# Kernel tuning notes

Hardware: AMD Instinct MI355X
Metric: run time of the kernel (lower is better)

The kernel has to match this reference:

```python
import jax, jax.numpy as jnp
import numpy as np

B, L, C, EW, H = 4, 512, 512, 64, 8
D = C // H          # dot_dim = 64
NI = 1024           # node ffn inner = round(512*2.0)
EI = 64             # edge ffn inner = round(64*1.0)
CLIP_LO, CLIP_HI = -5.0, 5.0


def _ln(x, g, b):
    m = jnp.mean(x, -1, keepdims=True)
    v = jnp.var(x, -1, keepdims=True)
    return (x - m) * jax.lax.rsqrt(v + 1e-5) * g + b


def setup_inputs() -> dict:
    key = jax.random.key(0)
    ks = iter(jax.random.split(key, 16))
    nrm = lambda shp: (0.02 * jax.random.normal(next(ks), shp)).astype(jnp.float32)
    z = lambda n: jnp.zeros((n,), jnp.float32)
    o = lambda n: jnp.ones((n,), jnp.float32)
    return {
        'h': jax.random.normal(next(ks), (B, L, C), jnp.float32),
        'e': jax.random.normal(next(ks), (B, L, L, EW), jnp.float32),
        'ln_h_g': o(C), 'ln_h_b': z(C),
        'ln_e_g': o(EW), 'ln_e_b': z(EW),
        'W_QKV': nrm((C, 3 * C)), 'b_QKV': z(3 * C),
        'W_E': nrm((EW, H)), 'b_E': z(H),
        'W_G': nrm((EW, H)), 'b_G': z(H),
        'W_Oh': nrm((C, C)), 'b_Oh': z(C),
        'ffn_ln_h_g': o(C), 'ffn_ln_h_b': z(C),
        'W_h1': nrm((C, NI)), 'b_h1': z(NI),
        'W_h2': nrm((NI, C)), 'b_h2': z(C),
        'W_Oe': nrm((H, EW)), 'b_Oe': z(EW),
        'ffn_ln_e_g': o(EW), 'ffn_ln_e_b': z(EW),
        'W_e1': nrm((EW, EI)), 'b_e1': z(EI),
        'W_e2': nrm((EI, EW)), 'b_e2': z(EW),
    }


def reference(h, e, ln_h_g, ln_h_b, ln_e_g, ln_e_b, W_QKV, b_QKV, W_E, b_E,
              W_G, b_G, W_Oh, b_Oh, ffn_ln_h_g, ffn_ln_h_b, W_h1, b_h1,
              W_h2, b_h2, W_Oe, b_Oe, ffn_ln_e_g, ffn_ln_e_b, W_e1, b_e1,
              W_e2, b_e2):
    h_ln = _ln(h, ln_h_g, ln_h_b)
    e_ln = _ln(e, ln_e_g, ln_e_b)
    QKV = h_ln @ W_QKV + b_QKV                    # [B,L,3C]
    E = e_ln @ W_E + b_E                          # [B,L,L,H]
    G = e_ln @ W_G + b_G                          # [B,L,L,H]
    qkv = QKV.reshape(B, L, 3 * D, H)             # torch view(B,L,-1,H)
    Q, K, V = qkv[:, :, :D], qkv[:, :, D:2 * D], qkv[:, :, 2 * D:]
    A_hat = jnp.einsum('bldh,bmdh->blmh', Q, K) * (D ** -0.5)
    H_hat = jnp.clip(A_hat, CLIP_LO, CLIP_HI) + E  # [B,L,L,H]
    gates = jax.nn.sigmoid(G)
    A_tild = jax.nn.softmax(H_hat, axis=2) * gates
    V_att = jnp.einsum('blmh,bmkh->blkh', A_tild, V)  # [B,L,D,H]
    deg = jnp.log1p(jnp.sum(gates, axis=2, keepdims=True))  # [B,L,1,H]
    V_att = (V_att * deg).reshape(B, L, C)
    # node MHA residual + FFN
    h1 = V_att @ W_Oh + b_Oh + h
    h_f = _ln(h1, ffn_ln_h_g, ffn_ln_h_b)
    h_out = h1 + (jax.nn.elu(h_f @ W_h1 + b_h1) @ W_h2 + b_h2)
    # edge MHA residual + FFN
    e1 = H_hat @ W_Oe + b_Oe + e
    e_f = _ln(e1, ffn_ln_e_g, ffn_ln_e_b)
    e_out = e1 + (jax.nn.elu(e_f @ W_e1 + b_e1) @ W_e2 + b_e2)
    return (h_out, e_out)
```

## Files before the change

### kernel.cpp

```cpp
#include <hip/hip_runtime.h>
#include <math.h>

typedef unsigned short u16t;
typedef unsigned int   u32t;
typedef __bf16 bf16x8 __attribute__((ext_vector_type(8)));
typedef float  f32x4  __attribute__((ext_vector_type(4)));

#define DEV static __device__ __forceinline__

DEV u16t bfc(float x){ u32t b=__float_as_uint(x); b += 0x7FFFu + ((b>>16)&1u); return (u16t)(b>>16); }
DEV float flc(u16t u){ return __uint_as_float(((u32t)u)<<16); }
DEV u32t pk2(u16t a, u16t b){ return (u32t)a | ((u32t)b<<16); }
DEV f32x4 fz4(){ f32x4 z = {0.f,0.f,0.f,0.f}; return z; }
DEV bf16x8 bz8(){ uint4 z = make_uint4(0u,0u,0u,0u); return __builtin_bit_cast(bf16x8, z); }
DEV f32x4 MFMA(bf16x8 a, bf16x8 b, f32x4 c){ return __builtin_amdgcn_mfma_f32_16x16x32_bf16(a,b,c,0,0,0); }

__global__ void kwTall(const float* __restrict__ A, u16t* __restrict__ oA,
                       const float* __restrict__ B, u16t* __restrict__ oB,
                       const float* __restrict__ C, u16t* __restrict__ oC,
                       const float* __restrict__ D, u16t* __restrict__ oD){
  int id = blockIdx.x*256 + threadIdx.x;
  if (id < 786432){ int n=id>>9, k=id&511; oA[id]=bfc(A[(size_t)k*1536+n]); return; }
  id -= 786432;
  if (id < 262144){ int n=id>>9, k=id&511; int ks=(k&63)*8+(k>>6); oB[id]=bfc(B[(size_t)ks*512+n]); return; }
  id -= 262144;
  if (id < 524288){ int n=id>>9, k=id&511; oC[id]=bfc(C[(size_t)k*1024+n]); return; }
  id -= 524288;
  { int n=id>>10, k=id&1023; oD[id]=bfc(D[(size_t)k*512+n]); }
}

__global__ __launch_bounds__(256) void kln(const float* __restrict__ in, const float* __restrict__ g,
                                           const float* __restrict__ b, u16t* __restrict__ out){
  int wv = threadIdx.x >> 6, lane = threadIdx.x & 63;
  int row = blockIdx.x*4 + wv;
  const float4* rp = reinterpret_cast<const float4*>(in + (size_t)row*512);
  float4 v0 = rp[lane], v1 = rp[lane+64];
  float s = v0.x+v0.y+v0.z+v0.w + v1.x+v1.y+v1.z+v1.w;
  float q = v0.x*v0.x+v0.y*v0.y+v0.z*v0.z+v0.w*v0.w + v1.x*v1.x+v1.y*v1.y+v1.z*v1.z+v1.w*v1.w;
  #pragma unroll
  for (int m=1;m<64;m<<=1){ s += __shfl_xor(s,m); q += __shfl_xor(q,m); }
  float mean = s*(1.f/512.f), var = q*(1.f/512.f)-mean*mean, rs = rsqrtf(var+1e-5f);
  const float4* gp = reinterpret_cast<const float4*>(g);
  const float4* bp = reinterpret_cast<const float4*>(b);
  float4 g0=gp[lane], g1=gp[lane+64], b0=bp[lane], b1=bp[lane+64];
  u16t* op = out + (size_t)row*512;
  ushort4 o0 = make_ushort4(bfc((v0.x-mean)*rs*g0.x+b0.x), bfc((v0.y-mean)*rs*g0.y+b0.y),
                            bfc((v0.z-mean)*rs*g0.z+b0.z), bfc((v0.w-mean)*rs*g0.w+b0.w));
  ushort4 o1 = make_ushort4(bfc((v1.x-mean)*rs*g1.x+b1.x), bfc((v1.y-mean)*rs*g1.y+b1.y),
                            bfc((v1.z-mean)*rs*g1.z+b1.z), bfc((v1.w-mean)*rs*g1.w+b1.w));
  reinterpret_cast<ushort4*>(op)[lane]    = o0;
  reinterpret_cast<ushort4*>(op)[lane+64] = o1;
}

__global__ __launch_bounds__(256) void kqkv(const u16t* __restrict__ hln, const u16t* __restrict__ Wt,
    const float* __restrict__ bias, u16t* __restrict__ Qb, u16t* __restrict__ Kb, u16t* __restrict__ Vt)
{
  __shared__ __align__(16) u16t As[16][520];
  __shared__ __align__(16) u16t Cs[16][1024];
  const int r0 = blockIdx.x*16, t = threadIdx.x;
  const int b8 = (r0 >> 9) * 8, pos0 = r0 & 511;
  {
    int row = t>>4, seg = t&15;
    const uint4* src = reinterpret_cast<const uint4*>(hln + (size_t)(r0+row)*512 + seg*32);
    uint4* dst = reinterpret_cast<uint4*>(&As[row][seg*32]);
    dst[0]=src[0]; dst[1]=src[1]; dst[2]=src[2]; dst[3]=src[3];
  }
  __syncthreads();
  const int wv = t>>6, lane = t&63;
  const int frow = lane&15, kgrp = (lane>>4)*8, rbase = (lane>>4)*4;
  for (int nt=0; nt<24; nt++){
    int n0 = (wv*24+nt)*16;
    f32x4 acc = fz4();
    for (int k0=0;k0<512;k0+=32){
      bf16x8 af = *reinterpret_cast<const bf16x8*>(&As[frow][k0+kgrp]);
      bf16x8 bf_ = *reinterpret_cast<const bf16x8*>(Wt + (size_t)(n0+frow)*512 + k0+kgrp);
      acc = MFMA(af,bf_,acc);
    }
    int col = n0 + frow;
    float bs = bias[col];
    if (n0 < 1024){
      #pragma unroll
      for (int r=0;r<4;r++) Cs[rbase+r][col] = bfc(acc[r]+bs);
    } else {
      int cc = col - 1024, dv = cc>>3, hq = cc&7;
      ushort4 u4 = make_ushort4(bfc(acc[0]+bs), bfc(acc[1]+bs), bfc(acc[2]+bs), bfc(acc[3]+bs));
      *reinterpret_cast<ushort4*>(Vt + ((size_t)(b8+hq)*64 + dv)*512 + pos0 + rbase) = u4;
    }
  }
  __syncthreads();
  {
    int pair = t>>1, halfq = t&1;
    int hq = pair>>4, lq = pair&15, d0 = halfq*32;
    int pos = pos0 + lq;
    u16t* qdst = Qb + ((size_t)(b8+hq)*512 + pos)*64 + d0;
    u16t* kdst = Kb + ((size_t)(b8+hq)*512 + pos)*64 + d0;
    #pragma unroll
    for (int v2=0; v2<4; v2++){
      uint4 u, uk;
      u.x  = pk2(Cs[lq][(d0+v2*8+0)*8+hq], Cs[lq][(d0+v2*8+1)*8+hq]);
      u.y  = pk2(Cs[lq][(d0+v2*8+2)*8+hq], Cs[lq][(d0+v2*8+3)*8+hq]);
      u.z  = pk2(Cs[lq][(d0+v2*8+4)*8+hq], Cs[lq][(d0+v2*8+5)*8+hq]);
      u.w  = pk2(Cs[lq][(d0+v2*8+6)*8+hq], Cs[lq][(d0+v2*8+7)*8+hq]);
      uk.x = pk2(Cs[lq][512+(d0+v2*8+0)*8+hq], Cs[lq][512+(d0+v2*8+1)*8+hq]);
      uk.y = pk2(Cs[lq][512+(d0+v2*8+2)*8+hq], Cs[lq][512+(d0+v2*8+3)*8+hq]);
      uk.z = pk2(Cs[lq][512+(d0+v2*8+4)*8+hq], Cs[lq][512+(d0+v2*8+5)*8+hq]);
      uk.w = pk2(Cs[lq][512+(d0+v2*8+6)*8+hq], Cs[lq][512+(d0+v2*8+7)*8+hq]);
      reinterpret_cast<uint4*>(qdst)[v2] = u;
      reinterpret_cast<uint4*>(kdst)[v2] = uk;
    }
  }
}

__global__ __launch_bounds__(512,4) void kattnF(
    const float* __restrict__ e, const float* __restrict__ lng, const float* __restrict__ lnb,
    const float* __restrict__ WE, const float* __restrict__ bE,
    const float* __restrict__ WG, const float* __restrict__ bG,
    const u16t* __restrict__ Qb, const u16t* __restrict__ Kb,
    const float* __restrict__ WOe, const float* __restrict__ bOe,
    const float* __restrict__ flg, const float* __restrict__ flb,
    const float* __restrict__ We1, const float* __restrict__ be1,
    const float* __restrict__ We2, const float* __restrict__ be2,
    u16t* __restrict__ Pg, float* __restrict__ Sp, float* __restrict__ Dp,
    float* __restrict__ eout)
{
  __shared__ __align__(16) u16t Eln[256][72];
  __shared__ u16t EGb[256][18];
  __shared__ __align__(16) u16t Hl[256][8];
  __shared__ __align__(16) u16t Pgs[16][8][16];
  __shared__ __align__(16) u16t WEGt[16][72];
  __shared__ __align__(16) u16t We1t[64][72];
  __shared__ __align__(16) u16t We2t[64][72];
  __shared__ __align__(16) u16t WOeT[64][8];
  __shared__ float lgs[64], lbs[64], flgs[64], flbs[64], bOes[64], be1s[64], be2s[64];
  __shared__ float bEs[8], bGs[8];

  const int t = threadIdx.x;
  const int b = blockIdx.z, lblk = blockIdx.x, chunk = blockIdx.y;
  const int l0 = lblk*16, m0g = chunk*128, b8 = b*8;

  if (t < 64){
    lgs[t]=lng[t]; lbs[t]=lnb[t]; flgs[t]=flg[t]; flbs[t]=flb[t];
    bOes[t]=bOe[t]; be1s[t]=be1[t]; be2s[t]=be2[t];
  }
  if (t < 8){ bEs[t]=bE[t]; bGs[t]=bG[t]; }
  for (int i=t; i<16*64; i+=512){
    int n = i>>6, k = i&63;
    WEGt[n][k] = bfc(n<8 ? WE[k*8+n] : WG[k*8+(n-8)]);
  }
  for (int i=t; i<4096; i+=512){
    int n=i>>6, k=i&63;
    We1t[n][k] = bfc(We1[k*64+n]);
    We2t[n][k] = bfc(We2[k*64+n]);
  }
  for (int i=t; i<512; i+=512){
    int n=i>>3, hh=i&7;
    WOeT[n][hh] = bfc(WOe[hh*64+n]);
  }
  __syncthreads();

  const int wv = t>>6, lane = t&63;
  const int frow = lane&15, kgrp = (lane>>4)*8, rbase = (lane>>4)*4;

  bf16x8 qf[2];
  #pragma unroll
  for (int kk=0;kk<2;kk++)
    qf[kk] = *reinterpret_cast<const bf16x8*>(Qb + ((size_t)(b8+wv)*512 + l0+frow)*64 + kk*32 + kgrp);

  float Ssum[4] = {0.f,0.f,0.f,0.f}, Dsum[4] = {0.f,0.f,0.f,0.f};

  const float* ebs[2];
  #pragma unroll
  for (int ti=0; ti<2; ti++)
    ebs[ti] = e + ((size_t)((b*512 + l0 + 2*wv+ti)*512) + m0g + frow)*64 + rbase;

  float4 xr[2][4];
  #pragma unroll
  for (int ti=0; ti<2; ti++)
    #pragma unroll
    for (int nb=0; nb<4; nb++)
      xr[ti][nb] = *reinterpret_cast<const float4*>(ebs[ti] + nb*16);

  #pragma unroll 1
  for (int mt=0; mt<8; mt++){
    const int m0 = m0g + mt*16;
    #pragma unroll
    for (int ti=0; ti<2; ti++){
      const int T = 2*wv + ti;
      float s_=0.f, q_=0.f;
      #pragma unroll
      for (int nb=0; nb<4; nb++){
        float4 v = xr[ti][nb];
        s_ += v.x+v.y+v.z+v.w;
        q_ += v.x*v.x+v.y*v.y+v.z*v.z+v.w*v.w;
      }
      s_ += __shfl_xor(s_,16); q_ += __shfl_xor(q_,16);
      s_ += __shfl_xor(s_,32); q_ += __shfl_xor(q_,32);
      float mean = s_*(1.f/64.f), var = q_*(1.f/64.f)-mean*mean, rs = rsqrtf(var+1e-5f);
      #pragma unroll
      for (int nb=0; nb<4; nb++){
        int n = nb*16 + rbase;
        float4 v = xr[ti][nb];
        uint2 uv;
        uv.x = pk2(bfc((v.x-mean)*rs*lgs[n  ]+lbs[n  ]), bfc((v.y-mean)*rs*lgs[n+1]+lbs[n+1]));
        uv.y = pk2(bfc((v.z-mean)*rs*lgs[n+2]+lbs[n+2]), bfc((v.w-mean)*rs*lgs[n+3]+lbs[n+3]));
        *reinterpret_cast<uint2*>(&Eln[T*16+frow][n]) = uv;
      }
    }
    #pragma unroll
    for (int ti=0; ti<2; ti++){
      int T = wv*2+ti;
      bf16x8 a0 = *reinterpret_cast<const bf16x8*>(&Eln[T*16+frow][kgrp]);
      bf16x8 a1 = *reinterpret_cast<const bf16x8*>(&Eln[T*16+frow][32+kgrp]);
      bf16x8 w0 = *reinterpret_cast<const bf16x8*>(&WEGt[frow][kgrp]);
      bf16x8 w1 = *reinterpret_cast<const bf16x8*>(&WEGt[frow][32+kgrp]);
      f32x4 acc = fz4(); acc = MFMA(a0,w0,acc); acc = MFMA(a1,w1,acc);
      #pragma unroll
      for (int r=0;r<4;r++) EGb[T*16+rbase+r][frow] = bfc(acc[r]);
    }
    __syncthreads();
    {
      const u16t* kb = Kb + ((size_t)(b8+wv)*512 + m0)*64 + frow*64 + kgrp;
      bf16x8 kf0 = *reinterpret_cast<const bf16x8*>(kb);
      bf16x8 kf1 = *reinterpret_cast<const bf16x8*>(kb + 32);
      f32x4 aq = fz4();
      aq = MFMA(qf[0], kf0, aq);
      aq = MFMA(qf[1], kf1, aq);
      #pragma unroll
      for (int r=0;r<4;r++){
        int lrow = rbase + r;
        int eidx = lrow*16 + frow;
        float ah = aq[r]*0.125f;
        ah = fminf(fmaxf(ah, -5.f), 5.f);
        float Ev = flc(EGb[eidx][wv])   + bEs[wv];
        float Gv = flc(EGb[eidx][8+wv]) + bGs[wv];
        float Hv = ah + Ev;
        float P = __expf(Hv);
        float g = 1.f/(1.f+__expf(-Gv));
        Ssum[r] += P; Dsum[r] += g;
        Hl[eidx][wv] = bfc(Hv);
        Pgs[lrow][wv][frow] = bfc(P*g);
      }
    }
    __syncthreads();
    if (t < 256){
      int lh = t>>1, half = t&1, l = lh>>3, h2 = lh&7;
      uint4 pv = *reinterpret_cast<const uint4*>(&Pgs[l][h2][half*8]);
      *reinterpret_cast<uint4*>(Pg + ((size_t)(b8+h2)*512 + l0+l)*512 + m0 + half*8) = pv;
    }
    #pragma unroll
    for (int ti=0; ti<2; ti++){
      const int T = 2*wv + ti;
      bf16x8 hf_ = bz8();
      if (kgrp==0) hf_ = *reinterpret_cast<const bf16x8*>(&Hl[T*16+frow][0]);
      f32x4 e1a[4];
      #pragma unroll
      for (int nb=0; nb<4; nb++){
        bf16x8 wf = bz8();
        if (kgrp==0) wf = *reinterpret_cast<const bf16x8*>(&WOeT[nb*16+frow][0]);
        e1a[nb] = MFMA(wf, hf_, fz4());
      }
      #pragma unroll
      for (int nb=0; nb<4; nb++){
        int n = nb*16 + rbase;
        e1a[nb][0] += bOes[n  ] + xr[ti][nb].x;
        e1a[nb][1] += bOes[n+1] + xr[ti][nb].y;
        e1a[nb][2] += bOes[n+2] + xr[ti][nb].z;
        e1a[nb][3] += bOes[n+3] + xr[ti][nb].w;
      }
      if (mt+1 < 8){
        #pragma unroll
        for (int nb=0; nb<4; nb++)
          xr[ti][nb] = *reinterpret_cast<const float4*>(ebs[ti] + (size_t)(mt+1)*16*64 + nb*16);
      }
      {
        float s_=0.f, q_=0.f;
        #pragma unroll
        for (int nb=0; nb<4; nb++){
          #pragma unroll
          for (int r=0;r<4;r++){ float v = e1a[nb][r]; s_ += v; q_ += v*v; }
        }
        s_ += __shfl_xor(s_,16); q_ += __shfl_xor(q_,16);
        s_ += __shfl_xor(s_,32); q_ += __shfl_xor(q_,32);
        float mean = s_*(1.f/64.f), var = q_*(1.f/64.f)-mean*mean, rs = rsqrtf(var+1e-5f);
        #pragma unroll
        for (int nb=0; nb<4; nb++){
          int n = nb*16 + rbase;
          uint2 uv;
          uv.x = pk2(bfc((e1a[nb][0]-mean)*rs*flgs[n  ]+flbs[n  ]), bfc((e1a[nb][1]-mean)*rs*flgs[n+1]+flbs[n+1]));
          uv.y = pk2(bfc((e1a[nb][2]-mean)*rs*flgs[n+2]+flbs[n+2]), bfc((e1a[nb][3]-mean)*rs*flgs[n+3]+flbs[n+3]));
          *reinterpret_cast<uint2*>(&Eln[T*16+frow][n]) = uv;
        }
      }
      {
        bf16x8 x0 = *reinterpret_cast<const bf16x8*>(&Eln[T*16+frow][kgrp]);
        bf16x8 x1 = *reinterpret_cast<const bf16x8*>(&Eln[T*16+frow][32+kgrp]);
        f32x4 acc1[4];
        #pragma unroll
        for (int nb=0;nb<4;nb++){
          bf16x8 w0 = *reinterpret_cast<const bf16x8*>(&We1t[nb*16+frow][kgrp]);
          bf16x8 w1 = *reinterpret_cast<const bf16x8*>(&We1t[nb*16+frow][32+kgrp]);
          f32x4 a_ = fz4(); a_ = MFMA(w0,x0,a_); a_ = MFMA(w1,x1,a_);
          acc1[nb] = a_;
        }
        #pragma unroll
        for (int nb=0;nb<4;nb++){
          int n = nb*16 + rbase;
          uint2 uv;
          float v0 = acc1[nb][0] + be1s[n  ]; v0 = v0>0.f ? v0 : (__expf(v0)-1.f);
          float v1 = acc1[nb][1] + be1s[n+1]; v1 = v1>0.f ? v1 : (__expf(v1)-1.f);
          float v2 = acc1[nb][2] + be1s[n+2]; v2 = v2>0.f ? v2 : (__expf(v2)-1.f);
          float v3 = acc1[nb][3] + be1s[n+3]; v3 = v3>0.f ? v3 : (__expf(v3)-1.f);
          uv.x = pk2(bfc(v0), bfc(v1));
          uv.y = pk2(bfc(v2), bfc(v3));
          *reinterpret_cast<uint2*>(&Eln[T*16+frow][n]) = uv;
        }
      }
      {
        bf16x8 x0 = *reinterpret_cast<const bf16x8*>(&Eln[T*16+frow][kgrp]);
        bf16x8 x1 = *reinterpret_cast<const bf16x8*>(&Eln[T*16+frow][32+kgrp]);
        float* eob = eout + ((size_t)((b*512 + l0 + T)*512) + m0 + frow)*64 + rbase;
        #pragma unroll
        for (int nb=0;nb<4;nb++){
          bf16x8 w0 = *reinterpret_cast<const bf16x8*>(&We2t[nb*16+frow][kgrp]);
          bf16x8 w1 = *reinterpret_cast<const bf16x8*>(&We2t[nb*16+frow][32+kgrp]);
          f32x4 a_ = fz4(); a_ = MFMA(w0,x0,a_); a_ = MFMA(w1,x1,a_);
          int n = nb*16 + rbase;
          float4 o;
          o.x = a_[0] + be2s[n  ] + e1a[nb][0];
          o.y = a_[1] + be2s[n+1] + e1a[nb][1];
          o.z = a_[2] + be2s[n+2] + e1a[nb][2];
          o.w = a_[3] + be2s[n+3] + e1a[nb][3];
          *reinterpret_cast<float4*>(eob + nb*16) = o;
        }
      }
    }
  }

  #pragma unroll
  for (int r=0;r<4;r++){
    float sv = Ssum[r], dv = Dsum[r];
    #pragma unroll
    for (int msk=1; msk<16; msk<<=1){ sv += __shfl_xor(sv, msk); dv += __shfl_xor(dv, msk); }
    int lrow = rbase + r;
    if (frow == 0){
      size_t idx = ((size_t)(b*512 + l0 + lrow)*8 + wv)*4 + chunk;
      Sp[idx] = sv; Dp[idx] = dv;
    }
  }
}

__global__ __launch_bounds__(256) void kpv(const u16t* __restrict__ Pg, const u16t* __restrict__ Vt,
    const float* __restrict__ Sp, const float* __restrict__ Dp, u16t* __restrict__ Va)
{
  const int bh = blockIdx.y, b = bh>>3, h = bh&7, l0 = blockIdx.x*16;
  const int b8 = b*8;
  __shared__ float scl[16];
  __shared__ __align__(16) u16t Vo[16][72];
  const int t = threadIdx.x;
  if (t < 16){
    const float* sp = Sp + ((size_t)(b*512 + l0+t)*8 + h)*4;
    const float* dp = Dp + ((size_t)(b*512 + l0+t)*8 + h)*4;
    float S = sp[0]+sp[1]+sp[2]+sp[3];
    float D = dp[0]+dp[1]+dp[2]+dp[3];
    scl[t] = log1pf(D)/S;
  }
  const int wv = t>>6, lane = t&63;
  const int frow = lane&15, kgrp = (lane>>4)*8, rbase = (lane>>4)*4;
  const u16t* pgb = Pg + ((size_t)(b8+h)*512 + l0)*512;
  const u16t* vb  = Vt + ((size_t)(b8+h)*64 + wv*16)*512;
  f32x4 acc = fz4();
  for (int k0=0;k0<512;k0+=32){
    bf16x8 a  = *reinterpret_cast<const bf16x8*>(pgb + (size_t)frow*512 + k0+kgrp);
    bf16x8 bf_= *reinterpret_cast<const bf16x8*>(vb  + (size_t)frow*512 + k0+kgrp);
    acc = MFMA(a,bf_,acc);
  }
  __syncthreads();
  #pragma unroll
  for (int r=0;r<4;r++) Vo[rbase+r][wv*16+frow] = bfc(acc[r]*scl[rbase+r]);
  __syncthreads();
  {
    int row = t>>4, c4 = t&15;
    *reinterpret_cast<uint2*>(Va + ((size_t)(b*512 + l0+row))*512 + h*64 + c4*4) =
      *reinterpret_cast<const uint2*>(&Vo[row][c4*4]);
  }
}

__global__ __launch_bounds__(256) void kgemmNS(const u16t* __restrict__ A, const u16t* __restrict__ Bt,
    const float* __restrict__ bias, const float* __restrict__ res,
    float* __restrict__ outf, u16t* __restrict__ outb, int N, int K, int do_elu)
{
  __shared__ __align__(16) u16t As[16][1032];
  const int r0 = blockIdx.x*16, t = threadIdx.x;
  {
    int row = t>>4, seg = t&15, cnt = K>>4;
    const uint4* src = reinterpret_cast<const uint4*>(A + (size_t)(r0+row)*K + seg*cnt);
    uint4* dst = reinterpret_cast<uint4*>(&As[row][seg*cnt]);
    for (int i=0;i<(cnt>>3);i++) dst[i] = src[i];
  }
  __syncthreads();
  const int wv = t>>6, lane = t&63;
  const int frow = lane&15, kgrp = (lane>>4)*8, rbase = (lane>>4)*4;
  int n0 = (blockIdx.y*4 + wv)*16;
  f32x4 acc = fz4();
  for (int k0=0;k0<K;k0+=32){
    bf16x8 af = *reinterpret_cast<const bf16x8*>(&As[frow][k0+kgrp]);
    bf16x8 bf_ = *reinterpret_cast<const bf16x8*>(Bt + (size_t)(n0+frow)*K + k0+kgrp);
    acc = MFMA(af,bf_,acc);
  }
  int col = n0 + frow;
  float bs = bias[col];
  #pragma unroll
  for (int r=0;r<4;r++){
    size_t row = (size_t)(r0 + rbase + r);
    float v = acc[r] + bs;
    if (do_elu) v = v>0.f ? v : (__expf(v)-1.f);
    if (res)  v += res[row*N + col];
    if (outf) outf[row*N + col] = v;
    if (outb) outb[row*N + col] = bfc(v);
  }
}

extern "C" void kernel_launch(void* const* d_in, const int* in_sizes, int n_in,
                              void* d_out, int out_size, void* d_ws, size_t ws_size,
                              hipStream_t stream)
{
  (void)in_sizes; (void)n_in; (void)out_size; (void)ws_size;
  const float* h      = (const float*)d_in[0];
  const float* e      = (const float*)d_in[1];
  const float* ln_h_g = (const float*)d_in[2];
  const float* ln_h_b = (const float*)d_in[3];
  const float* ln_e_g = (const float*)d_in[4];
  const float* ln_e_b = (const float*)d_in[5];
  const float* W_QKV  = (const float*)d_in[6];
  const float* b_QKV  = (const float*)d_in[7];
  const float* W_E    = (const float*)d_in[8];
  const float* b_E    = (const float*)d_in[9];
  const float* W_G    = (const float*)d_in[10];
  const float* b_G    = (const float*)d_in[11];
  const float* W_Oh   = (const float*)d_in[12];
  const float* b_Oh   = (const float*)d_in[13];
  const float* f_ln_h_g = (const float*)d_in[14];
  const float* f_ln_h_b = (const float*)d_in[15];
  const float* W_h1   = (const float*)d_in[16];
  const float* b_h1   = (const float*)d_in[17];
  const float* W_h2   = (const float*)d_in[18];
  const float* b_h2   = (const float*)d_in[19];
  const float* W_Oe   = (const float*)d_in[20];
  const float* b_Oe   = (const float*)d_in[21];
  const float* f_ln_e_g = (const float*)d_in[22];
  const float* f_ln_e_b = (const float*)d_in[23];
  const float* W_e1   = (const float*)d_in[24];
  const float* b_e1   = (const float*)d_in[25];
  const float* W_e2   = (const float*)d_in[26];
  const float* b_e2   = (const float*)d_in[27];

  float* out   = (float*)d_out;
  float* h_out = out;
  float* e_out = out + (size_t)4*512*512;

  char* w = (char*)d_ws;
  size_t off = 0;
  auto alloc = [&](size_t bytes)->char*{ char* p = w + off; off += (bytes + 255) & ~(size_t)255; return p; };
  u16t* hln   = (u16t*)alloc(2048ull*512*2);
  u16t* WtQKV = (u16t*)alloc(1536ull*512*2);
  u16t* WtOh  = (u16t*)alloc(512ull*512*2);
  u16t* WtH1  = (u16t*)alloc(1024ull*512*2);
  u16t* WtH2  = (u16t*)alloc(512ull*1024*2);
  u16t* Qb    = (u16t*)alloc(4ull*8*512*64*2);
  u16t* Kb    = (u16t*)alloc(4ull*8*512*64*2);
  u16t* Vt    = (u16t*)alloc(4ull*8*64*512*2);
  u16t* Pgb   = (u16t*)alloc(4ull*8*512*512*2);
  float* Sp   = (float*)alloc(4ull*512*8*4*4);
  float* Dp   = (float*)alloc(4ull*512*8*4*4);
  u16t* Va    = (u16t*)alloc(2048ull*512*2);
  float* h1   = (float*)alloc(2048ull*512*4);
  u16t* hfb   = (u16t*)alloc(2048ull*512*2);
  u16t* U     = (u16t*)alloc(2048ull*1024*2);

  kwTall<<<8192, 256, 0, stream>>>(W_QKV, WtQKV, W_Oh, WtOh, W_h1, WtH1, W_h2, WtH2);
  kln<<<512, 256, 0, stream>>>(h, ln_h_g, ln_h_b, hln);
  kqkv<<<128, 256, 0, stream>>>(hln, WtQKV, b_QKV, Qb, Kb, Vt);
  kattnF<<<dim3(32,4,4), 512, 0, stream>>>(e, ln_e_g, ln_e_b, W_E, b_E, W_G, b_G,
      Qb, Kb, W_Oe, b_Oe, f_ln_e_g, f_ln_e_b, W_e1, b_e1, W_e2, b_e2,
      Pgb, Sp, Dp, e_out);
  kpv<<<dim3(32,32), 256, 0, stream>>>(Pgb, Vt, Sp, Dp, Va);
  kgemmNS<<<dim3(128,8), 256, 0, stream>>>(Va, WtOh, b_Oh, h, h1, nullptr, 512, 512, 0);
  kln<<<512, 256, 0, stream>>>(h1, f_ln_h_g, f_ln_h_b, hfb);
  kgemmNS<<<dim3(128,16), 256, 0, stream>>>(hfb, WtH1, b_h1, nullptr, nullptr, U, 1024, 512, 1);
  kgemmNS<<<dim3(128,8), 256, 0, stream>>>(U, WtH2, b_h2, h1, h_out, nullptr, 512, 1024, 0);
}
```

Before: 395.0 us.

## Fuse P·V accumulation into attention kernel and drop Pg round-trip

```diff
diff --git a/kernel.cpp b/kernel.cpp
--- a/kernel.cpp
+++ b/kernel.cpp
@@ -111,22 +111,21 @@
   }
 }
 
-__global__ __launch_bounds__(512,4) void kattnF(
+__global__ __launch_bounds__(512,6) void kattnF(
     const float* __restrict__ e, const float* __restrict__ lng, const float* __restrict__ lnb,
     const float* __restrict__ WE, const float* __restrict__ bE,
     const float* __restrict__ WG, const float* __restrict__ bG,
-    const u16t* __restrict__ Qb, const u16t* __restrict__ Kb,
+    const u16t* __restrict__ Qb, const u16t* __restrict__ Kb, const u16t* __restrict__ Vt,
     const float* __restrict__ WOe, const float* __restrict__ bOe,
     const float* __restrict__ flg, const float* __restrict__ flb,
     const float* __restrict__ We1, const float* __restrict__ be1,
     const float* __restrict__ We2, const float* __restrict__ be2,
-    u16t* __restrict__ Pg, float* __restrict__ Sp, float* __restrict__ Dp,
+    u16t* __restrict__ Vp, float* __restrict__ Sp, float* __restrict__ Dp,
     float* __restrict__ eout)
 {
-  __shared__ __align__(16) u16t Eln[256][72];
-  __shared__ u16t EGb[256][18];
-  __shared__ __align__(16) u16t Hl[256][8];
-  __shared__ __align__(16) u16t Pgs[16][8][16];
+  __shared__ __align__(16) u16t Eln[128][72];
+  __shared__ __align__(16) u16t EG[128][20];
+  __shared__ __align__(16) u16t Pgs[8][8][16];
   __shared__ __align__(16) u16t WEGt[16][72];
   __shared__ __align__(16) u16t We1t[64][72];
   __shared__ __align__(16) u16t We2t[64][72];
@@ -136,14 +135,14 @@
 
   const int t = threadIdx.x;
   const int b = blockIdx.z, lblk = blockIdx.x, chunk = blockIdx.y;
-  const int l0 = lblk*16, m0g = chunk*128, b8 = b*8;
+  const int l0 = lblk*8, m0g = chunk*128, b8 = b*8;
 
   if (t < 64){
     lgs[t]=lng[t]; lbs[t]=lnb[t]; flgs[t]=flg[t]; flbs[t]=flb[t];
     bOes[t]=bOe[t]; be1s[t]=be1[t]; be2s[t]=be2[t];
   }
   if (t < 8){ bEs[t]=bE[t]; bGs[t]=bG[t]; }
-  for (int i=t; i<16*64; i+=512){
+  for (int i=t; i<1024; i+=512){
     int n = i>>6, k = i&63;
     WEGt[n][k] = bfc(n<8 ? WE[k*8+n] : WG[k*8+(n-8)]);
   }
@@ -152,8 +151,8 @@
     We1t[n][k] = bfc(We1[k*64+n]);
     We2t[n][k] = bfc(We2[k*64+n]);
   }
-  for (int i=t; i<512; i+=512){
-    int n=i>>3, hh=i&7;
+  {
+    int n=t>>3, hh=t&7;
     WOeT[n][hh] = bfc(WOe[hh*64+n]);
   }
   __syncthreads();
@@ -164,32 +163,28 @@
   bf16x8 qf[2];
   #pragma unroll
   for (int kk=0;kk<2;kk++)
-    qf[kk] = *reinterpret_cast<const bf16x8*>(Qb + ((size_t)(b8+wv)*512 + l0+frow)*64 + kk*32 + kgrp);
+    qf[kk] = (frow<8)
+      ? *reinterpret_cast<const bf16x8*>(Qb + ((size_t)(b8+wv)*512 + l0+frow)*64 + kk*32 + kgrp)
+      : bz8();
 
   float Ssum[4] = {0.f,0.f,0.f,0.f}, Dsum[4] = {0.f,0.f,0.f,0.f};
-
-  const float* ebs[2];
-  #pragma unroll
-  for (int ti=0; ti<2; ti++)
-    ebs[ti] = e + ((size_t)((b*512 + l0 + 2*wv+ti)*512) + m0g + frow)*64 + rbase;
-
-  float4 xr[2][4];
-  #pragma unroll
-  for (int ti=0; ti<2; ti++)
-    #pragma unroll
-    for (int nb=0; nb<4; nb++)
-      xr[ti][nb] = *reinterpret_cast<const float4*>(ebs[ti] + nb*16);
+  f32x4 accV[4];
+  #pragma unroll
+  for (int d=0;d<4;d++) accV[d]=fz4();
+
+  const float* ebs = e + ((size_t)((b*512 + l0 + wv)*512) + m0g + frow)*64 + rbase;
+  float4 xr[4];
+  #pragma unroll
+  for (int nb=0; nb<4; nb++) xr[nb] = *reinterpret_cast<const float4*>(ebs + nb*16);
 
   #pragma unroll 1
   for (int mt=0; mt<8; mt++){
     const int m0 = m0g + mt*16;
-    #pragma unroll
-    for (int ti=0; ti<2; ti++){
-      const int T = 2*wv + ti;
+    {
       float s_=0.f, q_=0.f;
       #pragma unroll
       for (int nb=0; nb<4; nb++){
-        float4 v = xr[ti][nb];
+        float4 v = xr[nb];
         s_ += v.x+v.y+v.z+v.w;
         q_ += v.x*v.x+v.y*v.y+v.z*v.z+v.w*v.w;
       }
@@ -199,23 +194,21 @@
       #pragma unroll
       for (int nb=0; nb<4; nb++){
         int n = nb*16 + rbase;
-        float4 v = xr[ti][nb];
+        float4 v = xr[nb];
         uint2 uv;
         uv.x = pk2(bfc((v.x-mean)*rs*lgs[n  ]+lbs[n  ]), bfc((v.y-mean)*rs*lgs[n+1]+lbs[n+1]));
         uv.y = pk2(bfc((v.z-mean)*rs*lgs[n+2]+lbs[n+2]), bfc((v.w-mean)*rs*lgs[n+3]+lbs[n+3]));
-        *reinterpret_cast<uint2*>(&Eln[T*16+frow][n]) = uv;
-      }
-    }
-    #pragma unroll
-    for (int ti=0; ti<2; ti++){
-      int T = wv*2+ti;
-      bf16x8 a0 = *reinterpret_cast<const bf16x8*>(&Eln[T*16+frow][kgrp]);
-      bf16x8 a1 = *reinterpret_cast<const bf16x8*>(&Eln[T*16+frow][32+kgrp]);
+        *reinterpret_cast<uint2*>(&Eln[wv*16+frow][n]) = uv;
+      }
+    }
+    {
+      bf16x8 a0 = *reinterpret_cast<const bf16x8*>(&Eln[wv*16+frow][kgrp]);
+      bf16x8 a1 = *reinterpret_cast<const bf16x8*>(&Eln[wv*16+frow][32+kgrp]);
       bf16x8 w0 = *reinterpret_cast<const bf16x8*>(&WEGt[frow][kgrp]);
       bf16x8 w1 = *reinterpret_cast<const bf16x8*>(&WEGt[frow][32+kgrp]);
       f32x4 acc = fz4(); acc = MFMA(a0,w0,acc); acc = MFMA(a1,w1,acc);
       #pragma unroll
-      for (int r=0;r<4;r++) EGb[T*16+rbase+r][frow] = bfc(acc[r]);
+      for (int r=0;r<4;r++) EG[wv*16+rbase+r][frow] = bfc(acc[r]);
     }
     __syncthreads();
     {
@@ -228,49 +221,62 @@
       #pragma unroll
       for (int r=0;r<4;r++){
         int lrow = rbase + r;
-        int eidx = lrow*16 + frow;
+        bool valid = (lrow < 8);
+        int eidx = (valid ? lrow : 0)*16 + frow;
         float ah = aq[r]*0.125f;
         ah = fminf(fmaxf(ah, -5.f), 5.f);
-        float Ev = flc(EGb[eidx][wv])   + bEs[wv];
-        float Gv = flc(EGb[eidx][8+wv]) + bGs[wv];
+        float Ev = flc(EG[eidx][wv])   + bEs[wv];
+        float Gv = flc(EG[eidx][8+wv]) + bGs[wv];
         float Hv = ah + Ev;
         float P = __expf(Hv);
         float g = 1.f/(1.f+__expf(-Gv));
+        if (!valid){ P=0.f; g=0.f; }
         Ssum[r] += P; Dsum[r] += g;
-        Hl[eidx][wv] = bfc(Hv);
-        Pgs[lrow][wv][frow] = bfc(P*g);
+        if (valid){
+          EG[eidx][wv] = bfc(Hv);
+          Pgs[wv][lrow][frow] = bfc(P*g);
+        }
       }
     }
     __syncthreads();
-    if (t < 256){
-      int lh = t>>1, half = t&1, l = lh>>3, h2 = lh&7;
-      uint4 pv = *reinterpret_cast<const uint4*>(&Pgs[l][h2][half*8]);
-      *reinterpret_cast<uint4*>(Pg + ((size_t)(b8+h2)*512 + l0+l)*512 + m0 + half*8) = pv;
-    }
-    #pragma unroll
-    for (int ti=0; ti<2; ti++){
-      const int T = 2*wv + ti;
+    {
+      bf16x8 pa = (frow<8 && kgrp<16)
+        ? *reinterpret_cast<const bf16x8*>(&Pgs[wv][frow][kgrp]) : bz8();
+      #pragma unroll
+      for (int db=0; db<4; db++){
+        bf16x8 vb = (kgrp<16)
+          ? *reinterpret_cast<const bf16x8*>(Vt + ((size_t)(b8+wv)*64 + db*16+frow)*512 + m0 + kgrp)
+          : bz8();
+        accV[db] = MFMA(pa, vb, accV[db]);
+      }
+    }
+    {
       bf16x8 hf_ = bz8();
-      if (kgrp==0) hf_ = *reinterpret_cast<const bf16x8*>(&Hl[T*16+frow][0]);
+      if (kgrp==0){
+        uint2 lo = *reinterpret_cast<const uint2*>(&EG[wv*16+frow][0]);
+        uint2 hi = *reinterpret_cast<const uint2*>(&EG[wv*16+frow][4]);
+        uint4 u; u.x=lo.x; u.y=lo.y; u.z=hi.x; u.w=hi.y;
+        hf_ = __builtin_bit_cast(bf16x8, u);
+      }
       f32x4 e1a[4];
       #pragma unroll
       for (int nb=0; nb<4; nb++){
         bf16x8 wf = bz8();
-        if (kgrp==0) wf = *reinterpret_cast<const bf16x8*>(&WOeT[nb*16+frow][0]);
+        if (kgrp==0) wf = *reinterpret_cast<const bf16x8*>(&WOeT[nb*16][0] + frow*8);
         e1a[nb] = MFMA(wf, hf_, fz4());
       }
       #pragma unroll
       for (int nb=0; nb<4; nb++){
         int n = nb*16 + rbase;
-        e1a[nb][0] += bOes[n  ] + xr[ti][nb].x;
-        e1a[nb][1] += bOes[n+1] + xr[ti][nb].y;
-        e1a[nb][2] += bOes[n+2] + xr[ti][nb].z;
-        e1a[nb][3] += bOes[n+3] + xr[ti][nb].w;
+        e1a[nb][0] += bOes[n  ] + xr[nb].x;
+        e1a[nb][1] += bOes[n+1] + xr[nb].y;
+        e1a[nb][2] += bOes[n+2] + xr[nb].z;
+        e1a[nb][3] += bOes[n+3] + xr[nb].w;
       }
       if (mt+1 < 8){
         #pragma unroll
         for (int nb=0; nb<4; nb++)
-          xr[ti][nb] = *reinterpret_cast<const float4*>(ebs[ti] + (size_t)(mt+1)*16*64 + nb*16);
+          xr[nb] = *reinterpret_cast<const float4*>(ebs + (size_t)(mt+1)*1024 + nb*16);
       }
       {
         float s_=0.f, q_=0.f;
@@ -288,12 +294,12 @@
           uint2 uv;
           uv.x = pk2(bfc((e1a[nb][0]-mean)*rs*flgs[n  ]+flbs[n  ]), bfc((e1a[nb][1]-mean)*rs*flgs[n+1]+flbs[n+1]));
           uv.y = pk2(bfc((e1a[nb][2]-mean)*rs*flgs[n+2]+flbs[n+2]), bfc((e1a[nb][3]-mean)*rs*flgs[n+3]+flbs[n+3]));
-          *reinterpret_cast<uint2*>(&Eln[T*16+frow][n]) = uv;
+          *reinterpret_cast<uint2*>(&Eln[wv*16+frow][n]) = uv;
         }
       }
       {
-        bf16x8 x0 = *reinterpret_cast<const bf16x8*>(&Eln[T*16+frow][kgrp]);
-        bf16x8 x1 = *reinterpret_cast<const bf16x8*>(&Eln[T*16+frow][32+kgrp]);
+        bf16x8 x0 = *reinterpret_cast<const bf16x8*>(&Eln[wv*16+frow][kgrp]);
+        bf16x8 x1 = *reinterpret_cast<const bf16x8*>(&Eln[wv*16+frow][32+kgrp]);
         f32x4 acc1[4];
         #pragma unroll
         for (int nb=0;nb<4;nb++){
@@ -305,20 +311,20 @@
         #pragma unroll
         for (int nb=0;nb<4;nb++){
           int n = nb*16 + rbase;
-          uint2 uv;
           float v0 = acc1[nb][0] + be1s[n  ]; v0 = v0>0.f ? v0 : (__expf(v0)-1.f);
           float v1 = acc1[nb][1] + be1s[n+1]; v1 = v1>0.f ? v1 : (__expf(v1)-1.f);
           float v2 = acc1[nb][2] + be1s[n+2]; v2 = v2>0.f ? v2 : (__expf(v2)-1.f);
           float v3 = acc1[nb][3] + be1s[n+3]; v3 = v3>0.f ? v3 : (__expf(v3)-1.f);
+          uint2 uv;
           uv.x = pk2(bfc(v0), bfc(v1));
           uv.y = pk2(bfc(v2), bfc(v3));
-          *reinterpret_cast<uint2*>(&Eln[T*16+frow][n]) = uv;
+          *reinterpret_cast<uint2*>(&Eln[wv*16+frow][n]) = uv;
         }
       }
       {
-        bf16x8 x0 = *reinterpret_cast<const bf16x8*>(&Eln[T*16+frow][kgrp]);
-        bf16x8 x1 = *reinterpret_cast<const bf16x8*>(&Eln[T*16+frow][32+kgrp]);
-        float* eob = eout + ((size_t)((b*512 + l0 + T)*512) + m0 + frow)*64 + rbase;
+        bf16x8 x0 = *reinterpret_cast<const bf16x8*>(&Eln[wv*16+frow][kgrp]);
+        bf16x8 x1 = *reinterpret_cast<const bf16x8*>(&Eln[wv*16+frow][32+kgrp]);
+        float* eob = eout + ((size_t)((b*512 + l0 + wv)*512) + m0 + frow)*64 + rbase;
         #pragma unroll
         for (int nb=0;nb<4;nb++){
           bf16x8 w0 = *reinterpret_cast<const bf16x8*>(&We2t[nb*16+frow][kgrp]);
@@ -342,47 +348,61 @@
     #pragma unroll
     for (int msk=1; msk<16; msk<<=1){ sv += __shfl_xor(sv, msk); dv += __shfl_xor(dv, msk); }
     int lrow = rbase + r;
-    if (frow == 0){
+    if (frow == 0 && lrow < 8){
       size_t idx = ((size_t)(b*512 + l0 + lrow)*8 + wv)*4 + chunk;
       Sp[idx] = sv; Dp[idx] = dv;
     }
   }
-}
-
-__global__ __launch_bounds__(256) void kpv(const u16t* __restrict__ Pg, const u16t* __restrict__ Vt,
+  __syncthreads();
+  float* Vo = reinterpret_cast<float*>(&Eln[0][0]);
+  if (kgrp < 16){
+    #pragma unroll
+    for (int db=0; db<4; db++){
+      #pragma unroll
+      for (int r=0;r<4;r++)
+        Vo[(size_t)(rbase+r)*512 + wv*64 + db*16 + frow] = accV[db][r];
+    }
+  }
+  __syncthreads();
+  {
+    int row = t>>6, i = t&63;
+    u16t* vpb = Vp + ((size_t)(chunk*2048 + b*512 + l0 + row))*512;
+    #pragma unroll
+    for (int j=0;j<2;j++){
+      int idx = (i + j*64)*4;
+      float4 f4 = *reinterpret_cast<const float4*>(&Vo[(size_t)row*512 + idx]);
+      uint2 o;
+      o.x = pk2(bfc(f4.x), bfc(f4.y));
+      o.y = pk2(bfc(f4.z), bfc(f4.w));
+      *reinterpret_cast<uint2*>(vpb + idx) = o;
+    }
+  }
+}
+
+__global__ __launch_bounds__(256) void kvfin(const u16t* __restrict__ Vp,
     const float* __restrict__ Sp, const float* __restrict__ Dp, u16t* __restrict__ Va)
 {
-  const int bh = blockIdx.y, b = bh>>3, h = bh&7, l0 = blockIdx.x*16;
-  const int b8 = b*8;
-  __shared__ float scl[16];
-  __shared__ __align__(16) u16t Vo[16][72];
+  const int row = blockIdx.x;
   const int t = threadIdx.x;
-  if (t < 16){
-    const float* sp = Sp + ((size_t)(b*512 + l0+t)*8 + h)*4;
-    const float* dp = Dp + ((size_t)(b*512 + l0+t)*8 + h)*4;
+  __shared__ float scl[8];
+  if (t < 8){
+    const float* sp = Sp + ((size_t)row*8 + t)*4;
+    const float* dp = Dp + ((size_t)row*8 + t)*4;
     float S = sp[0]+sp[1]+sp[2]+sp[3];
     float D = dp[0]+dp[1]+dp[2]+dp[3];
     scl[t] = log1pf(D)/S;
   }
-  const int wv = t>>6, lane = t&63;
-  const int frow = lane&15, kgrp = (lane>>4)*8, rbase = (lane>>4)*4;
-  const u16t* pgb = Pg + ((size_t)(b8+h)*512 + l0)*512;
-  const u16t* vb  = Vt + ((size_t)(b8+h)*64 + wv*16)*512;
-  f32x4 acc = fz4();
-  for (int k0=0;k0<512;k0+=32){
-    bf16x8 a  = *reinterpret_cast<const bf16x8*>(pgb + (size_t)frow*512 + k0+kgrp);
-    bf16x8 bf_= *reinterpret_cast<const bf16x8*>(vb  + (size_t)frow*512 + k0+kgrp);
-    acc = MFMA(a,bf_,acc);
-  }
-  __syncthreads();
-  #pragma unroll
-  for (int r=0;r<4;r++) Vo[rbase+r][wv*16+frow] = bfc(acc[r]*scl[rbase+r]);
-  __syncthreads();
-  {
-    int row = t>>4, c4 = t&15;
-    *reinterpret_cast<uint2*>(Va + ((size_t)(b*512 + l0+row))*512 + h*64 + c4*4) =
-      *reinterpret_cast<const uint2*>(&Vo[row][c4*4]);
-  }
+  __syncthreads();
+  int c = t*2;
+  float v0=0.f, v1=0.f;
+  #pragma unroll
+  for (int ch=0; ch<4; ch++){
+    u32t u = *reinterpret_cast<const u32t*>(Vp + ((size_t)(ch*2048 + row))*512 + c);
+    v0 += flc((u16t)(u & 0xffffu));
+    v1 += flc((u16t)(u >> 16));
+  }
+  float s = scl[c>>6];
+  *reinterpret_cast<u32t*>(Va + (size_t)row*512 + c) = pk2(bfc(v0*s), bfc(v1*s));
 }
 
 __global__ __launch_bounds__(256) void kgemmNS(const u16t* __restrict__ A, const u16t* __restrict__ Bt,
@@ -469,7 +489,7 @@
   u16t* Qb    = (u16t*)alloc(4ull*8*512*64*2);
   u16t* Kb    = (u16t*)alloc(4ull*8*512*64*2);
   u16t* Vt    = (u16t*)alloc(4ull*8*64*512*2);
-  u16t* Pgb   = (u16t*)alloc(4ull*8*512*512*2);
+  u16t* Vp    = (u16t*)alloc(4ull*2048*512*2);
   float* Sp   = (float*)alloc(4ull*512*8*4*4);
   float* Dp   = (float*)alloc(4ull*512*8*4*4);
   u16t* Va    = (u16t*)alloc(2048ull*512*2);
@@ -480,10 +500,10 @@
   kwTall<<<8192, 256, 0, stream>>>(W_QKV, WtQKV, W_Oh, WtOh, W_h1, WtH1, W_h2, WtH2);
   kln<<<512, 256, 0, stream>>>(h, ln_h_g, ln_h_b, hln);
   kqkv<<<128, 256, 0, stream>>>(hln, WtQKV, b_QKV, Qb, Kb, Vt);
-  kattnF<<<dim3(32,4,4), 512, 0, stream>>>(e, ln_e_g, ln_e_b, W_E, b_E, W_G, b_G,
-      Qb, Kb, W_Oe, b_Oe, f_ln_e_g, f_ln_e_b, W_e1, b_e1, W_e2, b_e2,
-      Pgb, Sp, Dp, e_out);
-  kpv<<<dim3(32,32), 256, 0, stream>>>(Pgb, Vt, Sp, Dp, Va);
+  kattnF<<<dim3(64,4,4), 512, 0, stream>>>(e, ln_e_g, ln_e_b, W_E, b_E, W_G, b_G,
+      Qb, Kb, Vt, W_Oe, b_Oe, f_ln_e_g, f_ln_e_b, W_e1, b_e1, W_e2, b_e2,
+      Vp, Sp, Dp, e_out);
+  kvfin<<<2048, 256, 0, stream>>>(Vp, Sp, Dp, Va);
   kgemmNS<<<dim3(128,8), 256, 0, stream>>>(Va, WtOh, b_Oh, h, h1, nullptr, 512, 512, 0);
   kln<<<512, 256, 0, stream>>>(h1, f_ln_h_g, f_ln_h_b, hfb);
   kgemmNS<<<dim3(128,16), 256, 0, stream>>>(hfb, WtH1, b_h1, nullptr, nullptr, U, 1024, 512, 1);
```

New measurement: 729.2 us. 84.6% more time.

## Fuse P·V product into attention kernel with per-chunk partial outputs

Applied to the files above, without the earlier changes.

```diff
diff --git a/kernel.cpp b/kernel.cpp
--- a/kernel.cpp
+++ b/kernel.cpp
@@ -3,12 +3,14 @@
 
 typedef unsigned short u16t;
 typedef unsigned int   u32t;
+typedef __bf16 bf16x2 __attribute__((ext_vector_type(2)));
 typedef __bf16 bf16x8 __attribute__((ext_vector_type(8)));
 typedef float  f32x4  __attribute__((ext_vector_type(4)));
 
 #define DEV static __device__ __forceinline__
 
-DEV u16t bfc(float x){ u32t b=__float_as_uint(x); b += 0x7FFFu + ((b>>16)&1u); return (u16t)(b>>16); }
+DEV u16t bfc(float x){ __bf16 b = (__bf16)x; return __builtin_bit_cast(u16t, b); }
+DEV u32t pkbf(float a, float b){ bf16x2 v = {(__bf16)a, (__bf16)b}; return __builtin_bit_cast(u32t, v); }
 DEV float flc(u16t u){ return __uint_as_float(((u32t)u)<<16); }
 DEV u32t pk2(u16t a, u16t b){ return (u32t)a | ((u32t)b<<16); }
 DEV f32x4 fz4(){ f32x4 z = {0.f,0.f,0.f,0.f}; return z; }
@@ -44,12 +46,13 @@
   const float4* bp = reinterpret_cast<const float4*>(b);
   float4 g0=gp[lane], g1=gp[lane+64], b0=bp[lane], b1=bp[lane+64];
   u16t* op = out + (size_t)row*512;
-  ushort4 o0 = make_ushort4(bfc((v0.x-mean)*rs*g0.x+b0.x), bfc((v0.y-mean)*rs*g0.y+b0.y),
-                            bfc((v0.z-mean)*rs*g0.z+b0.z), bfc((v0.w-mean)*rs*g0.w+b0.w));
-  ushort4 o1 = make_ushort4(bfc((v1.x-mean)*rs*g1.x+b1.x), bfc((v1.y-mean)*rs*g1.y+b1.y),
-                            bfc((v1.z-mean)*rs*g1.z+b1.z), bfc((v1.w-mean)*rs*g1.w+b1.w));
-  reinterpret_cast<ushort4*>(op)[lane]    = o0;
-  reinterpret_cast<ushort4*>(op)[lane+64] = o1;
+  uint2 o0, o1;
+  o0.x = pkbf((v0.x-mean)*rs*g0.x+b0.x, (v0.y-mean)*rs*g0.y+b0.y);
+  o0.y = pkbf((v0.z-mean)*rs*g0.z+b0.z, (v0.w-mean)*rs*g0.w+b0.w);
+  o1.x = pkbf((v1.x-mean)*rs*g1.x+b1.x, (v1.y-mean)*rs*g1.y+b1.y);
+  o1.y = pkbf((v1.z-mean)*rs*g1.z+b1.z, (v1.w-mean)*rs*g1.w+b1.w);
+  reinterpret_cast<uint2*>(op)[lane]    = o0;
+  reinterpret_cast<uint2*>(op)[lane+64] = o1;
 }
 
 __global__ __launch_bounds__(256) void kqkv(const u16t* __restrict__ hln, const u16t* __restrict__ Wt,
@@ -115,12 +118,12 @@
     const float* __restrict__ e, const float* __restrict__ lng, const float* __restrict__ lnb,
     const float* __restrict__ WE, const float* __restrict__ bE,
     const float* __restrict__ WG, const float* __restrict__ bG,
-    const u16t* __restrict__ Qb, const u16t* __restrict__ Kb,
+    const u16t* __restrict__ Qb, const u16t* __restrict__ Kb, const u16t* __restrict__ Vt,
     const float* __restrict__ WOe, const float* __restrict__ bOe,
     const float* __restrict__ flg, const float* __restrict__ flb,
     const float* __restrict__ We1, const float* __restrict__ be1,
     const float* __restrict__ We2, const float* __restrict__ be2,
-    u16t* __restrict__ Pg, float* __restrict__ Sp, float* __restrict__ Dp,
+    u16t* __restrict__ Vp, float* __restrict__ Sp, float* __restrict__ Dp,
     float* __restrict__ eout)
 {
   __shared__ __align__(16) u16t Eln[256][72];
@@ -143,7 +146,7 @@
     bOes[t]=bOe[t]; be1s[t]=be1[t]; be2s[t]=be2[t];
   }
   if (t < 8){ bEs[t]=bE[t]; bGs[t]=bG[t]; }
-  for (int i=t; i<16*64; i+=512){
+  for (int i=t; i<1024; i+=512){
     int n = i>>6, k = i&63;
     WEGt[n][k] = bfc(n<8 ? WE[k*8+n] : WG[k*8+(n-8)]);
   }
@@ -152,8 +155,8 @@
     We1t[n][k] = bfc(We1[k*64+n]);
     We2t[n][k] = bfc(We2[k*64+n]);
   }
-  for (int i=t; i<512; i+=512){
-    int n=i>>3, hh=i&7;
+  {
+    int n=t>>3, hh=t&7;
     WOeT[n][hh] = bfc(WOe[hh*64+n]);
   }
   __syncthreads();
@@ -167,6 +170,9 @@
     qf[kk] = *reinterpret_cast<const bf16x8*>(Qb + ((size_t)(b8+wv)*512 + l0+frow)*64 + kk*32 + kgrp);
 
   float Ssum[4] = {0.f,0.f,0.f,0.f}, Dsum[4] = {0.f,0.f,0.f,0.f};
+  f32x4 accV[4];
+  #pragma unroll
+  for (int d=0;d<4;d++) accV[d]=fz4();
 
   const float* ebs[2];
   #pragma unroll
@@ -201,8 +207,8 @@
         int n = nb*16 + rbase;
         float4 v = xr[ti][nb];
         uint2 uv;
-        uv.x = pk2(bfc((v.x-mean)*rs*lgs[n  ]+lbs[n  ]), bfc((v.y-mean)*rs*lgs[n+1]+lbs[n+1]));
-        uv.y = pk2(bfc((v.z-mean)*rs*lgs[n+2]+lbs[n+2]), bfc((v.w-mean)*rs*lgs[n+3]+lbs[n+3]));
+        uv.x = pkbf((v.x-mean)*rs*lgs[n  ]+lbs[n  ], (v.y-mean)*rs*lgs[n+1]+lbs[n+1]);
+        uv.y = pkbf((v.z-mean)*rs*lgs[n+2]+lbs[n+2], (v.w-mean)*rs*lgs[n+3]+lbs[n+3]);
         *reinterpret_cast<uint2*>(&Eln[T*16+frow][n]) = uv;
       }
     }
@@ -241,12 +247,18 @@
         Pgs[lrow][wv][frow] = bfc(P*g);
       }
     }
+    {
+      bf16x8 pa = (kgrp<16)
+        ? *reinterpret_cast<const bf16x8*>(&Pgs[frow][wv][kgrp]) : bz8();
+      #pragma unroll
+      for (int db=0; db<4; db++){
+        bf16x8 vb = (kgrp<16)
+          ? *reinterpret_cast<const bf16x8*>(Vt + ((size_t)(b8+wv)*64 + db*16+frow)*512 + m0 + kgrp)
+          : bz8();
+        accV[db] = MFMA(pa, vb, accV[db]);
+      }
+    }
     __syncthreads();
-    if (t < 256){
-      int lh = t>>1, half = t&1, l = lh>>3, h2 = lh&7;
-      uint4 pv = *reinterpret_cast<const uint4*>(&Pgs[l][h2][half*8]);
-      *reinterpret_cast<uint4*>(Pg + ((size_t)(b8+h2)*512 + l0+l)*512 + m0 + half*8) = pv;
-    }
     #pragma unroll
     for (int ti=0; ti<2; ti++){
       const int T = 2*wv + ti;
@@ -256,7 +268,7 @@
       #pragma unroll
       for (int nb=0; nb<4; nb++){
         bf16x8 wf = bz8();
-        if (kgrp==0) wf = *reinterpret_cast<const bf16x8*>(&WOeT[nb*16+frow][0]);
+        if (kgrp==0) wf = *reinterpret_cast<const bf16x8*>(&WOeT[nb*16][0] + frow*8);
         e1a[nb] = MFMA(wf, hf_, fz4());
       }
       #pragma unroll
@@ -270,7 +282,7 @@
       if (mt+1 < 8){
         #pragma unroll
         for (int nb=0; nb<4; nb++)
-          xr[ti][nb] = *reinterpret_cast<const float4*>(ebs[ti] + (size_t)(mt+1)*16*64 + nb*16);
+          xr[ti][nb] = *reinterpret_cast<const float4*>(ebs[ti] + (size_t)(mt+1)*1024 + nb*16);
       }
       {
         float s_=0.f, q_=0.f;
@@ -286,8 +298,8 @@
         for (int nb=0; nb<4; nb++){
           int n = nb*16 + rbase;
           uint2 uv;
-          uv.x = pk2(bfc((e1a[nb][0]-mean)*rs*flgs[n  ]+flbs[n  ]), bfc((e1a[nb][1]-mean)*rs*flgs[n+1]+flbs[n+1]));
-          uv.y = pk2(bfc((e1a[nb][2]-mean)*rs*flgs[n+2]+flbs[n+2]), bfc((e1a[nb][3]-mean)*rs*flgs[n+3]+flbs[n+3]));
+          uv.x = pkbf((e1a[nb][0]-mean)*rs*flgs[n  ]+flbs[n  ], (e1a[nb][1]-mean)*rs*flgs[n+1]+flbs[n+1]);
+          uv.y = pkbf((e1a[nb][2]-mean)*rs*flgs[n+2]+flbs[n+2], (e1a[nb][3]-mean)*rs*flgs[n+3]+flbs[n+3]);
           *reinterpret_cast<uint2*>(&Eln[T*16+frow][n]) = uv;
         }
       }
@@ -305,13 +317,13 @@
         #pragma unroll
         for (int nb=0;nb<4;nb++){
           int n = nb*16 + rbase;
-          uint2 uv;
           float v0 = acc1[nb][0] + be1s[n  ]; v0 = v0>0.f ? v0 : (__expf(v0)-1.f);
           float v1 = acc1[nb][1] + be1s[n+1]; v1 = v1>0.f ? v1 : (__expf(v1)-1.f);
           float v2 = acc1[nb][2] + be1s[n+2]; v2 = v2>0.f ? v2 : (__expf(v2)-1.f);
           float v3 = acc1[nb][3] + be1s[n+3]; v3 = v3>0.f ? v3 : (__expf(v3)-1.f);
-          uv.x = pk2(bfc(v0), bfc(v1));
-          uv.y = pk2(bfc(v2), bfc(v3));
+          uint2 uv;
+          uv.x = pkbf(v0, v1);
+          uv.y = pkbf(v2, v3);
           *reinterpret_cast<uint2*>(&Eln[T*16+frow][n]) = uv;
         }
       }
@@ -347,42 +359,53 @@
       Sp[idx] = sv; Dp[idx] = dv;
     }
   }
-}
-
-__global__ __launch_bounds__(256) void kpv(const u16t* __restrict__ Pg, const u16t* __restrict__ Vt,
+  __syncthreads();
+  float* Vo = reinterpret_cast<float*>(&Eln[0][0]);
+  #pragma unroll
+  for (int db=0; db<4; db++){
+    #pragma unroll
+    for (int r=0;r<4;r++)
+      Vo[(size_t)(rbase+r)*512 + wv*64 + db*16 + frow] = accV[db][r];
+  }
+  __syncthreads();
+  {
+    int row = t>>5, i = t&31;
+    u16t* vpb = Vp + ((size_t)(chunk*2048 + b*512 + l0 + row))*512 + i*16;
+    const float* vsrc = &Vo[(size_t)row*512 + i*16];
+    uint4 o0, o1;
+    o0.x = pkbf(vsrc[0],  vsrc[1]);  o0.y = pkbf(vsrc[2],  vsrc[3]);
+    o0.z = pkbf(vsrc[4],  vsrc[5]);  o0.w = pkbf(vsrc[6],  vsrc[7]);
+    o1.x = pkbf(vsrc[8],  vsrc[9]);  o1.y = pkbf(vsrc[10], vsrc[11]);
+    o1.z = pkbf(vsrc[12], vsrc[13]); o1.w = pkbf(vsrc[14], vsrc[15]);
+    reinterpret_cast<uint4*>(vpb)[0] = o0;
+    reinterpret_cast<uint4*>(vpb)[1] = o1;
+  }
+}
+
+__global__ __launch_bounds__(256) void kvfin(const u16t* __restrict__ Vp,
     const float* __restrict__ Sp, const float* __restrict__ Dp, u16t* __restrict__ Va)
 {
-  const int bh = blockIdx.y, b = bh>>3, h = bh&7, l0 = blockIdx.x*16;
-  const int b8 = b*8;
-  __shared__ float scl[16];
-  __shared__ __align__(16) u16t Vo[16][72];
+  const int row = blockIdx.x;
   const int t = threadIdx.x;
-  if (t < 16){
-    const float* sp = Sp + ((size_t)(b*512 + l0+t)*8 + h)*4;
-    const float* dp = Dp + ((size_t)(b*512 + l0+t)*8 + h)*4;
+  __shared__ float scl[8];
+  if (t < 8){
+    const float* sp = Sp + ((size_t)row*8 + t)*4;
+    const float* dp = Dp + ((size_t)row*8 + t)*4;
     float S = sp[0]+sp[1]+sp[2]+sp[3];
     float D = dp[0]+dp[1]+dp[2]+dp[3];
     scl[t] = log1pf(D)/S;
   }
-  const int wv = t>>6, lane = t&63;
-  const int frow = lane&15, kgrp = (lane>>4)*8, rbase = (lane>>4)*4;
-  const u16t* pgb = Pg + ((size_t)(b8+h)*512 + l0)*512;
-  const u16t* vb  = Vt + ((size_t)(b8+h)*64 + wv*16)*512;
-  f32x4 acc = fz4();
-  for (int k0=0;k0<512;k0+=32){
-    bf16x8 a  = *reinterpret_cast<const bf16x8*>(pgb + (size_t)frow*512 + k0+kgrp);
-    bf16x8 bf_= *reinterpret_cast<const bf16x8*>(vb  + (size_t)frow*512 + k0+kgrp);
-    acc = MFMA(a,bf_,acc);
-  }
-  __syncthreads();
-  #pragma unroll
-  for (int r=0;r<4;r++) Vo[rbase+r][wv*16+frow] = bfc(acc[r]*scl[rbase+r]);
-  __syncthreads();
-  {
-    int row = t>>4, c4 = t&15;
-    *reinterpret_cast<uint2*>(Va + ((size_t)(b*512 + l0+row))*512 + h*64 + c4*4) =
-      *reinterpret_cast<const uint2*>(&Vo[row][c4*4]);
-  }
+  __syncthreads();
+  int c = t*2;
+  float v0=0.f, v1=0.f;
+  #pragma unroll
+  for (int ch=0; ch<4; ch++){
+    u32t u = *reinterpret_cast<const u32t*>(Vp + ((size_t)(ch*2048 + row))*512 + c);
+    v0 += flc((u16t)(u & 0xffffu));
+    v1 += flc((u16t)(u >> 16));
+  }
+  float s = scl[c>>6];
+  *reinterpret_cast<u32t*>(Va + (size_t)row*512 + c) = pkbf(v0*s, v1*s);
 }
 
 __global__ __launch_bounds__(256) void kgemmNS(const u16t* __restrict__ A, const u16t* __restrict__ Bt,
@@ -469,7 +492,7 @@
   u16t* Qb    = (u16t*)alloc(4ull*8*512*64*2);
   u16t* Kb    = (u16t*)alloc(4ull*8*512*64*2);
   u16t* Vt    = (u16t*)alloc(4ull*8*64*512*2);
-  u16t* Pgb   = (u16t*)alloc(4ull*8*512*512*2);
+  u16t* Vp    = (u16t*)alloc(4ull*2048*512*2);
   float* Sp   = (float*)alloc(4ull*512*8*4*4);
   float* Dp   = (float*)alloc(4ull*512*8*4*4);
   u16t* Va    = (u16t*)alloc(2048ull*512*2);
@@ -481,9 +504,9 @@
   kln<<<512, 256, 0, stream>>>(h, ln_h_g, ln_h_b, hln);
   kqkv<<<128, 256, 0, stream>>>(hln, WtQKV, b_QKV, Qb, Kb, Vt);
   kattnF<<<dim3(32,4,4), 512, 0, stream>>>(e, ln_e_g, ln_e_b, W_E, b_E, W_G, b_G,
-      Qb, Kb, W_Oe, b_Oe, f_ln_e_g, f_ln_e_b, W_e1, b_e1, W_e2, b_e2,
-      Pgb, Sp, Dp, e_out);
-  kpv<<<dim3(32,32), 256, 0, stream>>>(Pgb, Vt, Sp, Dp, Va);
+      Qb, Kb, Vt, W_Oe, b_Oe, f_ln_e_g, f_ln_e_b, W_e1, b_e1, W_e2, b_e2,
+      Vp, Sp, Dp, e_out);
+  kvfin<<<2048, 256, 0, stream>>>(Vp, Sp, Dp, Va);
   kgemmNS<<<dim3(128,8), 256, 0, stream>>>(Va, WtOh, b_Oh, h, h1, nullptr, 512, 512, 0);
   kln<<<512, 256, 0, stream>>>(h1, f_ln_h_g, f_ln_h_b, hfb);
   kgemmNS<<<dim3(128,16), 256, 0, stream>>>(hfb, WtH1, b_h1, nullptr, nullptr, U, 1024, 512, 1);
```

Result: faster. 383.8 us (-2.8%).
